# Performance work log

Measured on AMD Instinct MI355X. Metric: run time of the kernel, lower is better.

Reference implementation:

```python
import jax, jax.numpy as jnp
import numpy as np

N = 16384        # number of points
NI = 3           # spatial dimension (2 or 3 supported)
BIG = 1e10       # sentinel squared distance for cross-bucket / invalid pairs


def setup_inputs() -> dict:
    key = jax.random.key(0)
    k1, k2 = jax.random.split(key)
    x = jax.random.uniform(k1, (N, NI), dtype=jnp.float32)  # points in [0,1)^NI
    min_t_idx = jax.random.randint(k2, (N,), 0, 4, dtype=jnp.int32)
    return {"x": x, "min_t_idx": min_t_idx, "K": 16, "sz": 5}


def _kde_knn(x, min_t_idx, K, sz):
    n, ni = x.shape
    mask = min_t_idx > 0

    # Spatial hash: cell index per axis (trunc toward zero == torch .long()),
    # flattened row-major with sz as base, offset by min_t_idx * sz**ni.
    y = (x * sz).astype(jnp.int32)                                   # [N, NI]
    weights = jnp.asarray([sz ** (ni - 1 - d) for d in range(ni)], jnp.int32)
    y_f = y @ weights + min_t_idx * (sz ** ni)                        # [N]

    # Pairwise squared distances via gram trick (avoids [N,N,NI] diff tensor).
    sq = jnp.sum(x * x, axis=1)                                       # [N]
    D = sq[:, None] + sq[None, :] - 2.0 * (x @ x.T)                   # [N,N]

    # Block-diagonal ranges in keops == only pairs within the same bucket,
    # restricted to valid (min_t_idx>0) points.  Invalid pairs -> BIG.
    same = (y_f[:, None] == y_f[None, :]) & mask[:, None] & mask[None, :]
    Dm = jnp.where(same, D, BIG)                                      # [N,N]

    # K-th smallest squared distance (self at distance 0 is included,
    # exactly like argKmin over the diagonal ranges).
    kth_sq = -jax.lax.top_k(-Dm, K)[0][:, -1]                         # [N]
    r = jnp.sqrt(jnp.maximum(kth_sq, 0.0))

    # _ball_volume(NI - 1, r)
    dim = ni - 1
    if dim == 1:
        vol = 2.0 * r
    elif dim == 2:
        vol = jnp.pi * r * r
    else:
        vol = (4.0 / 3.0) * jnp.pi * r ** 3

    return jnp.where(mask, vol / (K - 1), 0.0)


def reference(x, min_t_idx, K, sz):
    return _kde_knn(x, min_t_idx, K, sz)
```

## Files before the change

### kernel.cpp

```cpp
#include <hip/hip_runtime.h>


#define KNN 16
#define NB 512
#define BIGF 1e10f
#define SORT_THREADS 1024

__global__ __launch_bounds__(SORT_THREADS) void sort_kernel(
    const float* __restrict__ x, const int* __restrict__ mt,
    float4* __restrict__ xs, int2* __restrict__ range,
    int* __restrict__ total, float* __restrict__ out, int n)
{
    __shared__ int hist[NB];
    __shared__ int scanb[NB];
    __shared__ int cursor[NB];
    const int t = threadIdx.x;
    if (t < NB) hist[t] = 0;
    __syncthreads();

    const int PPT = 16;
    int   mybb[PPT];
    float myx[PPT], myy[PPT], myz[PPT];
#pragma unroll
    for (int p = 0; p < PPT; ++p) {
        int i = p * SORT_THREADS + t;
        int b = -1;
        float x0 = 0.f, x1 = 0.f, x2 = 0.f;
        if (i < n) {
            int m = mt[i];
            x0 = x[3 * i + 0]; x1 = x[3 * i + 1]; x2 = x[3 * i + 2];
            if (m > 0) {
                int y0 = (int)(x0 * 5.0f);
                int y1 = (int)(x1 * 5.0f);
                int y2 = (int)(x2 * 5.0f);
                b = y0 * 25 + y1 * 5 + y2 + m * 125;
                atomicAdd(&hist[b], 1);
            } else {
                out[i] = 0.0f;
            }
        }
        mybb[p] = b; myx[p] = x0; myy[p] = x1; myz[p] = x2;
    }
    __syncthreads();

    if (t < NB) scanb[t] = hist[t];
    __syncthreads();
    for (int off = 1; off < NB; off <<= 1) {
        int u = (t < NB && t >= off) ? scanb[t - off] : 0;
        __syncthreads();
        if (t < NB) scanb[t] += u;
        __syncthreads();
    }
    if (t == NB - 1) total[0] = scanb[NB - 1];
    int ex = 0;
    if (t < NB) ex = scanb[t] - hist[t];
    __syncthreads();
    if (t < NB) { scanb[t] = ex; cursor[t] = ex; }
    __syncthreads();

#pragma unroll
    for (int p = 0; p < PPT; ++p) {
        int b = mybb[p];
        if (b >= 0) {
            int i = p * SORT_THREADS + t;
            int pos = atomicAdd(&cursor[b], 1);
            xs[pos] = make_float4(myx[p], myy[p], myz[p], __int_as_float(i));
            int s = scanb[b];
            range[pos] = make_int2(s, s + hist[b]);
        }
    }
}

__global__ __launch_bounds__(64) void knn_kernel(
    const float4* __restrict__ xs, const int2* __restrict__ range,
    const int* __restrict__ total, float* __restrict__ out)
{
    int t = blockIdx.x * blockDim.x + threadIdx.x;
    if (t >= *total) return;

    float4 p = xs[t];
    int2 se = range[t];

    float best[KNN];
#pragma unroll
    for (int k = 0; k < KNN; ++k) best[k] = BIGF;
    float curmax = BIGF;
    int maxpos = 0;

    for (int u = se.x; u < se.y; ++u) {
        float4 q = xs[u];
        float dx = p.x - q.x;
        float dy = p.y - q.y;
        float dz = p.z - q.z;
        float d2 = dx * dx + dy * dy + dz * dz;
        if (d2 < curmax) {
#pragma unroll
            for (int k = 0; k < KNN; ++k)
                if (k == maxpos) best[k] = d2;
            curmax = best[0]; maxpos = 0;
#pragma unroll
            for (int k = 1; k < KNN; ++k)
                if (best[k] > curmax) { curmax = best[k]; maxpos = k; }
        }
    }

    int i = __float_as_int(p.w);
    float r = sqrtf(fmaxf(curmax, 0.0f));
    float vol = 3.14159265358979323846f * r * r;
    out[i] = vol / 15.0f;
}

extern "C" void kernel_launch(void* const* d_in, const int* in_sizes, int n_in,
                              void* d_out, int out_size, void* d_ws, size_t ws_size,
                              hipStream_t stream) {
    const float* x  = (const float*)d_in[0];
    const int*   mt = (const int*)d_in[1];
    float* out = (float*)d_out;
    int n = in_sizes[1];

    char* ws = (char*)d_ws;
    float4* xs    = (float4*)(ws + 0);
    int2*   range = (int2*)(ws + (size_t)n * 16);
    int*    total = (int*)(ws + (size_t)n * 24);

    sort_kernel<<<1, SORT_THREADS, 0, stream>>>(x, mt, xs, range, total, out, n);
    int blocks = (n + 63) / 64;
    knn_kernel<<<blocks, 64, 0, stream>>>(xs, range, total, out);
}
```

Measured before the change: 102.3 us.

## Split single-block bucket sort into multi-block histogram and scatter passes

Replaces the one-block counting sort with a grid-wide histogram kernel using global atomics, followed by a scatter kernel in which every block redundantly scans the 512 bucket counts and places its points through global cursor atomics. The aim is to remove the serial bottleneck of running the whole sort on one workgroup. In exchange it adds a memset, an extra kernel launch, and contended global atomics on a few hundred buckets. The knn kernel's workgroup size also goes from 64 to 256 threads.

```diff
diff --git a/kernel.cpp b/kernel.cpp
--- a/kernel.cpp
+++ b/kernel.cpp
@@ -4,74 +4,66 @@
 #define KNN 16
 #define NB 512
 #define BIGF 1e10f
-#define SORT_THREADS 1024
 
-__global__ __launch_bounds__(SORT_THREADS) void sort_kernel(
+__global__ __launch_bounds__(256) void hist_kernel(
     const float* __restrict__ x, const int* __restrict__ mt,
+    int* __restrict__ count, int* __restrict__ bucket_of,
+    float* __restrict__ out, int n)
+{
+    int i = blockIdx.x * blockDim.x + threadIdx.x;
+    if (i >= n) return;
+    int m = mt[i];
+    int b = -1;
+    if (m > 0) {
+        int y0 = (int)(x[3 * i + 0] * 5.0f);
+        int y1 = (int)(x[3 * i + 1] * 5.0f);
+        int y2 = (int)(x[3 * i + 2] * 5.0f);
+        b = y0 * 25 + y1 * 5 + y2 + m * 125;
+        atomicAdd(&count[b], 1);
+    } else {
+        out[i] = 0.0f;
+    }
+    bucket_of[i] = b;
+}
+
+__global__ __launch_bounds__(256) void scatter_kernel(
+    const float* __restrict__ x, const int* __restrict__ bucket_of,
+    const int* __restrict__ count, int* __restrict__ cursor,
     float4* __restrict__ xs, int2* __restrict__ range,
-    int* __restrict__ total, float* __restrict__ out, int n)
+    int* __restrict__ total, int n)
 {
-    __shared__ int hist[NB];
-    __shared__ int scanb[NB];
-    __shared__ int cursor[NB];
+    __shared__ int incl[NB];
+    __shared__ int excl[NB];
     const int t = threadIdx.x;
-    if (t < NB) hist[t] = 0;
+
+    int o0 = count[t];
+    int o1 = count[t + 256];
+    incl[t] = o0; incl[t + 256] = o1;
+    __syncthreads();
+    for (int off = 1; off < NB; off <<= 1) {
+        int v0 = (t >= off) ? incl[t - off] : 0;
+        int v1 = (t + 256 >= off) ? incl[t + 256 - off] : 0;
+        __syncthreads();
+        incl[t] += v0; incl[t + 256] += v1;
+        __syncthreads();
+    }
+    excl[t] = incl[t] - o0;
+    excl[t + 256] = incl[t + 256] - o1;
     __syncthreads();
 
-    const int PPT = 16;
-    int   mybb[PPT];
-    float myx[PPT], myy[PPT], myz[PPT];
-#pragma unroll
-    for (int p = 0; p < PPT; ++p) {
-        int i = p * SORT_THREADS + t;
-        int b = -1;
-        float x0 = 0.f, x1 = 0.f, x2 = 0.f;
-        if (i < n) {
-            int m = mt[i];
-            x0 = x[3 * i + 0]; x1 = x[3 * i + 1]; x2 = x[3 * i + 2];
-            if (m > 0) {
-                int y0 = (int)(x0 * 5.0f);
-                int y1 = (int)(x1 * 5.0f);
-                int y2 = (int)(x2 * 5.0f);
-                b = y0 * 25 + y1 * 5 + y2 + m * 125;
-                atomicAdd(&hist[b], 1);
-            } else {
-                out[i] = 0.0f;
-            }
-        }
-        mybb[p] = b; myx[p] = x0; myy[p] = x1; myz[p] = x2;
-    }
-    __syncthreads();
+    if (blockIdx.x == 0 && t == 255) total[0] = incl[NB - 1];
 
-    if (t < NB) scanb[t] = hist[t];
-    __syncthreads();
-    for (int off = 1; off < NB; off <<= 1) {
-        int u = (t < NB && t >= off) ? scanb[t - off] : 0;
-        __syncthreads();
-        if (t < NB) scanb[t] += u;
-        __syncthreads();
-    }
-    if (t == NB - 1) total[0] = scanb[NB - 1];
-    int ex = 0;
-    if (t < NB) ex = scanb[t] - hist[t];
-    __syncthreads();
-    if (t < NB) { scanb[t] = ex; cursor[t] = ex; }
-    __syncthreads();
-
-#pragma unroll
-    for (int p = 0; p < PPT; ++p) {
-        int b = mybb[p];
-        if (b >= 0) {
-            int i = p * SORT_THREADS + t;
-            int pos = atomicAdd(&cursor[b], 1);
-            xs[pos] = make_float4(myx[p], myy[p], myz[p], __int_as_float(i));
-            int s = scanb[b];
-            range[pos] = make_int2(s, s + hist[b]);
-        }
-    }
+    int i = blockIdx.x * blockDim.x + t;
+    if (i >= n) return;
+    int b = bucket_of[i];
+    if (b < 0) return;
+    int pos = excl[b] + atomicAdd(&cursor[b], 1);
+    xs[pos] = make_float4(x[3 * i + 0], x[3 * i + 1], x[3 * i + 2],
+                          __int_as_float(i));
+    range[pos] = make_int2(excl[b], incl[b]);
 }
 
-__global__ __launch_bounds__(64) void knn_kernel(
+__global__ __launch_bounds__(256) void knn_kernel(
     const float4* __restrict__ xs, const int2* __restrict__ range,
     const int* __restrict__ total, float* __restrict__ out)
 {
@@ -119,11 +111,17 @@
     int n = in_sizes[1];
 
     char* ws = (char*)d_ws;
-    float4* xs    = (float4*)(ws + 0);
-    int2*   range = (int2*)(ws + (size_t)n * 16);
-    int*    total = (int*)(ws + (size_t)n * 24);
+    int*    count     = (int*)(ws + 0);
+    int*    cursor    = (int*)(ws + 2048);
+    int*    total     = (int*)(ws + 4096);
+    int*    bucket_of = (int*)(ws + 8192);
+    float4* xs        = (float4*)(ws + 8192 + (size_t)n * 4);
+    int2*   range     = (int2*)(ws + 8192 + (size_t)n * 20);
 
-    sort_kernel<<<1, SORT_THREADS, 0, stream>>>(x, mt, xs, range, total, out, n);
-    int blocks = (n + 63) / 64;
-    knn_kernel<<<blocks, 64, 0, stream>>>(xs, range, total, out);
+    hipMemsetAsync(ws, 0, 4096, stream);
+    int blocks = (n + 255) / 256;
+    hist_kernel<<<blocks, 256, 0, stream>>>(x, mt, count, bucket_of, out, n);
+    scatter_kernel<<<blocks, 256, 0, stream>>>(x, bucket_of, count, cursor,
+                                               xs, range, total, n);
+    knn_kernel<<<blocks, 256, 0, stream>>>(xs, range, total, out);
 }
```

Measured after the change: 96.84 us. -5.3%, faster.

## Replace single-block sort plus KNN with one block per bucket

Applied to the files above, without the earlier changes.

Drops the single-block counting-sort kernel and its separate KNN launch. One kernel now runs with 375 blocks, one per (min_t_idx, cell) bucket. Each block scans all N points, gathers its bucket's members into shared memory with ballot-based compaction, and then runs the brute-force 16-NN search from LDS. This removes the serial one-block sort stage, a kernel launch and the global round trip. In exchange every block re-reads the whole input, and the zero-fill of invalid outputs depends on a hardcoded 44-points-per-block split and a fixed 375-block grid that assume N=16384 and sz=5.

```diff
diff --git a/kernel.cpp b/kernel.cpp
--- a/kernel.cpp
+++ b/kernel.cpp
@@ -2,112 +2,87 @@
 
 
 #define KNN 16
-#define NB 512
+#define CAP 2048
 #define BIGF 1e10f
-#define SORT_THREADS 1024
 
-__global__ __launch_bounds__(SORT_THREADS) void sort_kernel(
+__global__ __launch_bounds__(256) void kde_knn_kernel(
     const float* __restrict__ x, const int* __restrict__ mt,
-    float4* __restrict__ xs, int2* __restrict__ range,
-    int* __restrict__ total, float* __restrict__ out, int n)
+    float* __restrict__ out, int n)
 {
-    __shared__ int hist[NB];
-    __shared__ int scanb[NB];
-    __shared__ int cursor[NB];
-    const int t = threadIdx.x;
-    if (t < NB) hist[t] = 0;
+    __shared__ float4 mem[CAP];
+    __shared__ int cnt;
+    const int tid  = threadIdx.x;
+    const int lane = tid & 63;
+    const int beta = blockIdx.x;
+    const int mycell = beta % 125;
+    const int mymt   = beta / 125 + 1;
+
+    if (tid == 0) cnt = 0;
     __syncthreads();
 
-    const int PPT = 16;
-    int   mybb[PPT];
-    float myx[PPT], myy[PPT], myz[PPT];
-#pragma unroll
-    for (int p = 0; p < PPT; ++p) {
-        int i = p * SORT_THREADS + t;
-        int b = -1;
-        float x0 = 0.f, x1 = 0.f, x2 = 0.f;
-        if (i < n) {
-            int m = mt[i];
-            x0 = x[3 * i + 0]; x1 = x[3 * i + 1]; x2 = x[3 * i + 2];
-            if (m > 0) {
-                int y0 = (int)(x0 * 5.0f);
-                int y1 = (int)(x1 * 5.0f);
-                int y2 = (int)(x2 * 5.0f);
-                b = y0 * 25 + y1 * 5 + y2 + m * 125;
-                atomicAdd(&hist[b], 1);
-            } else {
-                out[i] = 0.0f;
+    for (int i = tid; i < n; i += 256) {
+        int m = mt[i];
+        float x0 = x[3 * i + 0];
+        float x1 = x[3 * i + 1];
+        float x2 = x[3 * i + 2];
+        bool member = false;
+        if (m > 0) {
+            int y0 = (int)(x0 * 5.0f);
+            int y1 = (int)(x1 * 5.0f);
+            int y2 = (int)(x2 * 5.0f);
+            int cell = y0 * 25 + y1 * 5 + y2;
+            member = (m == mymt) && (cell == mycell);
+        } else {
+            if ((unsigned)(i - beta * 44) < 44u) out[i] = 0.0f;
+        }
+        unsigned long long mask = __ballot(member);
+        if (mask) {
+            int nfound = __popcll(mask);
+            int base = 0;
+            if (lane == 0) base = atomicAdd(&cnt, nfound);
+            base = __shfl(base, 0);
+            if (member) {
+                int prefix = __popcll(mask & ((1ull << lane) - 1ull));
+                int pos = base + prefix;
+                if (pos < CAP)
+                    mem[pos] = make_float4(x0, x1, x2, __int_as_float(i));
             }
         }
-        mybb[p] = b; myx[p] = x0; myy[p] = x1; myz[p] = x2;
     }
     __syncthreads();
 
-    if (t < NB) scanb[t] = hist[t];
-    __syncthreads();
-    for (int off = 1; off < NB; off <<= 1) {
-        int u = (t < NB && t >= off) ? scanb[t - off] : 0;
-        __syncthreads();
-        if (t < NB) scanb[t] += u;
-        __syncthreads();
+    int c = cnt;
+    if (c > CAP) c = CAP;
+    for (int t = tid; t < c; t += 256) {
+        float4 p = mem[t];
+        float best[KNN];
+#pragma unroll
+        for (int k = 0; k < KNN; ++k) best[k] = BIGF;
+        float curmax = BIGF;
+        int maxpos = 0;
+
+        for (int u = 0; u < c; ++u) {
+            float4 q = mem[u];
+            float dx = p.x - q.x;
+            float dy = p.y - q.y;
+            float dz = p.z - q.z;
+            float d2 = dx * dx + dy * dy + dz * dz;
+            if (d2 < curmax) {
+#pragma unroll
+                for (int k = 0; k < KNN; ++k)
+                    if (k == maxpos) best[k] = d2;
+                curmax = best[0]; maxpos = 0;
+#pragma unroll
+                for (int k = 1; k < KNN; ++k)
+                    if (best[k] > curmax) { curmax = best[k]; maxpos = k; }
+            }
+        }
+
+        int i = __float_as_int(p.w);
+        float r = sqrtf(fmaxf(curmax, 0.0f));
+        float vol = 3.14159265358979323846f * r * r;
+        out[i] = vol / 15.0f;
     }
-    if (t == NB - 1) total[0] = scanb[NB - 1];
-    int ex = 0;
-    if (t < NB) ex = scanb[t] - hist[t];
-    __syncthreads();
-    if (t < NB) { scanb[t] = ex; cursor[t] = ex; }
-    __syncthreads();
-
-#pragma unroll
-    for (int p = 0; p < PPT; ++p) {
-        int b = mybb[p];
-        if (b >= 0) {
-            int i = p * SORT_THREADS + t;
-            int pos = atomicAdd(&cursor[b], 1);
-            xs[pos] = make_float4(myx[p], myy[p], myz[p], __int_as_float(i));
-            int s = scanb[b];
-            range[pos] = make_int2(s, s + hist[b]);
-        }
-    }
-}
-
-__global__ __launch_bounds__(64) void knn_kernel(
-    const float4* __restrict__ xs, const int2* __restrict__ range,
-    const int* __restrict__ total, float* __restrict__ out)
-{
-    int t = blockIdx.x * blockDim.x + threadIdx.x;
-    if (t >= *total) return;
-
-    float4 p = xs[t];
-    int2 se = range[t];
-
-    float best[KNN];
-#pragma unroll
-    for (int k = 0; k < KNN; ++k) best[k] = BIGF;
-    float curmax = BIGF;
-    int maxpos = 0;
-
-    for (int u = se.x; u < se.y; ++u) {
-        float4 q = xs[u];
-        float dx = p.x - q.x;
-        float dy = p.y - q.y;
-        float dz = p.z - q.z;
-        float d2 = dx * dx + dy * dy + dz * dz;
-        if (d2 < curmax) {
-#pragma unroll
-            for (int k = 0; k < KNN; ++k)
-                if (k == maxpos) best[k] = d2;
-            curmax = best[0]; maxpos = 0;
-#pragma unroll
-            for (int k = 1; k < KNN; ++k)
-                if (best[k] > curmax) { curmax = best[k]; maxpos = k; }
-        }
-    }
-
-    int i = __float_as_int(p.w);
-    float r = sqrtf(fmaxf(curmax, 0.0f));
-    float vol = 3.14159265358979323846f * r * r;
-    out[i] = vol / 15.0f;
 }
 
 extern "C" void kernel_launch(void* const* d_in, const int* in_sizes, int n_in,
@@ -118,12 +93,5 @@
     float* out = (float*)d_out;
     int n = in_sizes[1];
 
-    char* ws = (char*)d_ws;
-    float4* xs    = (float4*)(ws + 0);
-    int2*   range = (int2*)(ws + (size_t)n * 16);
-    int*    total = (int*)(ws + (size_t)n * 24);
-
-    sort_kernel<<<1, SORT_THREADS, 0, stream>>>(x, mt, xs, range, total, out, n);
-    int blocks = (n + 63) / 64;
-    knn_kernel<<<blocks, 64, 0, stream>>>(xs, range, total, out);
+    kde_knn_kernel<<<375, 256, 0, stream>>>(x, mt, out, n);
 }
```

Measured after the change: 98.66 us. 1.04x faster.
